# Optimization experiments

Measured on AMD Instinct MI355X. Metric: run time of the kernel, lower is better.

## Reference

```python
import jax, jax.numpy as jnp
import numpy as np

N, K, C, S = 40000, 16, 128, 8  # points, neighbors, channels, share_planes
EPS = 1e-5


def _bn(x, g, b, m, v):
    # eval-mode BatchNorm1d over the channel (last) axis
    return (x - m) * (g * jax.lax.rsqrt(v + EPS)) + b


def _forward(xyz, feats, Wq, bq, Wk, bk, Wv, bv, Wp1, bp1, p_gamma, p_beta, p_mean, p_var,
             Wp2, bp2, w_gamma, w_beta, w_mean, w_var, Ww1, bw1, w1_gamma, w1_beta,
             w1_mean, w1_var, Ww2, bw2, nei_ind):
    x = feats[0]          # (N, C)
    pos = xyz[0]          # (N, 3)
    idx = nei_ind[0]      # (N, K)

    q = x @ Wq + bq                      # (N, C)
    kf = (x @ Wk + bk)[idx]              # (N, K, C) neighbor gather
    vf = (x @ Wv + bv)[idx]              # (N, K, C)

    d = pos[idx] - pos[:, None, :]       # (N, K, 3) relative positions
    # linear_p: Linear_BN(3,3) -> ReLU -> Linear(3, C)
    p = jax.nn.relu(_bn(d @ Wp1 + bp1, p_gamma, p_beta, p_mean, p_var)) @ Wp2 + bp2  # (N, K, C)

    # mid_planes == out_planes, so the view(...,1,mid).sum(2) is an identity reshape
    w = kf - q[:, None, :] + p           # (N, K, C)
    w = _bn(w, w_gamma, w_beta, w_mean, w_var)  # bn_w over channels
    # linear_w: ReLU -> Linear_BN(C, C//S) -> ReLU -> Linear(C//S, C//S)
    w = jax.nn.relu(_bn(jax.nn.relu(w) @ Ww1 + bw1, w1_gamma, w1_beta, w1_mean, w1_var)) @ Ww2 + bw2  # (N, K, C//S)
    w = jax.nn.softmax(w, axis=1)        # softmax over K neighbors

    # grouped-channel weighted sum over neighbors
    agg = ((vf + p).reshape(N, K, S, C // S) * w[:, :, None, :]).sum(axis=1).reshape(N, C)

    # shortcut is Identity (in_planes == out_planes); broadcast over batch dim like torch
    return jax.nn.leaky_relu(agg[None, :, :] + feats, negative_slope=0.1)  # (1, N, C)


def setup_inputs() -> dict:
    key = jax.random.key(0)
    ks = jax.random.split(key, 16)
    f32 = jnp.float32

    def w(k, shape, scale):
        return jax.random.normal(k, shape, dtype=f32) * scale

    return {
        "xyz": jax.random.uniform(ks[0], (1, N, 3), dtype=f32),
        "feats": jax.random.normal(ks[1], (1, N, C), dtype=f32),
        "nei_ind": jax.random.randint(ks[2], (1, N, K), 0, N, dtype=jnp.int32),
        "Wq": w(ks[3], (C, C), C ** -0.5), "bq": jnp.zeros((C,), f32),
        "Wk": w(ks[4], (C, C), C ** -0.5), "bk": jnp.zeros((C,), f32),
        "Wv": w(ks[5], (C, C), C ** -0.5), "bv": jnp.zeros((C,), f32),
        "Wp1": w(ks[6], (3, 3), 0.5), "bp1": jnp.zeros((3,), f32),
        "p_gamma": jnp.ones((3,), f32), "p_beta": jnp.zeros((3,), f32),
        "p_mean": w(ks[7], (3,), 0.1), "p_var": jnp.ones((3,), f32),
        "Wp2": w(ks[8], (3, C), 0.5), "bp2": jnp.zeros((C,), f32),
        "w_gamma": jnp.ones((C,), f32), "w_beta": jnp.zeros((C,), f32),
        "w_mean": w(ks[9], (C,), 0.1), "w_var": jnp.ones((C,), f32),
        "Ww1": w(ks[10], (C, C // S), C ** -0.5), "bw1": jnp.zeros((C // S,), f32),
        "w1_gamma": jnp.ones((C // S,), f32), "w1_beta": jnp.zeros((C // S,), f32),
        "w1_mean": w(ks[11], (C // S,), 0.1), "w1_var": jnp.ones((C // S,), f32),
        "Ww2": w(ks[12], (C // S, C // S), (C // S) ** -0.5), "bw2": jnp.zeros((C // S,), f32),
    }


def reference(xyz, feats, nei_ind, Wq, bq, Wk, bk, Wv, bv, Wp1, bp1, p_gamma, p_beta,
              p_mean, p_var, Wp2, bp2, w_gamma, w_beta, w_mean, w_var, Ww1, bw1,
              w1_gamma, w1_beta, w1_mean, w1_var, Ww2, bw2):
    return _forward(xyz, feats, Wq, bq, Wk, bk, Wv, bv, Wp1, bp1, p_gamma, p_beta,
                    p_mean, p_var, Wp2, bp2, w_gamma, w_beta, w_mean, w_var, Ww1, bw1,
                    w1_gamma, w1_beta, w1_mean, w1_var, Ww2, bw2, nei_ind)
```

## Files before the change

kernel.cpp:

```cpp
#include <hip/hip_runtime.h>
#include <stdint.h>

#define N_PTS 40000
#define KNBR  16
#define CH    128
#define EPSV  1e-5f

typedef __attribute__((ext_vector_type(4))) float f32x4;
typedef __attribute__((ext_vector_type(8))) short bf16x8;

__device__ __forceinline__ float bf2f(ushort u) {
    union { uint32_t i; float f; } x; x.i = ((uint32_t)u) << 16; return x.f;
}
__device__ __forceinline__ float bflo(uint32_t u) {
    union { uint32_t i; float f; } x; x.i = u << 16; return x.f;
}
__device__ __forceinline__ float bfhi(uint32_t u) {
    union { uint32_t i; float f; } x; x.i = u & 0xffff0000u; return x.f;
}
__device__ __forceinline__ ushort f2bf(float f) {
    union { float f; uint32_t i; } x; x.f = f;
    uint32_t i = x.i;
    i += 0x7fffu + ((i >> 16) & 1u);
    return (ushort)(i >> 16);
}

#if __has_builtin(__builtin_amdgcn_cvt_pk_bf16_f32)
typedef __bf16 bf16x2v __attribute__((ext_vector_type(2)));
__device__ __forceinline__ uint32_t pack2(float a, float b) {
    union { bf16x2v v; uint32_t u; } x;
    x.v = __builtin_amdgcn_cvt_pk_bf16_f32(a, b);
    return x.u;
}
#else
__device__ __forceinline__ uint32_t pack2(float a, float b) {
    return (uint32_t)f2bf(a) | ((uint32_t)f2bf(b) << 16);
}
#endif

template <bool BF> struct IO;
template <> struct IO<true> {
    static __device__ __forceinline__ float  ld (const void* p, int i) { return bf2f(((const ushort*)p)[i]); }
    static __device__ __forceinline__ float2 ld2(const void* p, int i) { const uint32_t u = ((const uint32_t*)p)[i]; return make_float2(bflo(u), bfhi(u)); }
    static __device__ __forceinline__ ushort ldbf(const void* p, int i) { return ((const ushort*)p)[i]; }
    static __device__ __forceinline__ void   st2(void* p, int i, float a, float b) { ((uint32_t*)p)[i] = pack2(a, b); }
};
template <> struct IO<false> {
    static __device__ __forceinline__ float  ld (const void* p, int i) { return ((const float*)p)[i]; }
    static __device__ __forceinline__ float2 ld2(const void* p, int i) { return ((const float2*)p)[i]; }
    static __device__ __forceinline__ ushort ldbf(const void* p, int i) { return f2bf(((const float*)p)[i]); }
    static __device__ __forceinline__ void   st2(void* p, int i, float a, float b) { ((float2*)p)[i] = make_float2(a, b); }
};

__device__ __forceinline__ bool detect_bf16(const void* w_var) {
    return (*(const uint32_t*)w_var & 0xffffu) != 0u;
}

template <bool BF>
__device__ void wtrans_body(const void* Wq, const void* Wk, const void* Wv,
                            ushort* wt)
{
    const int m    = blockIdx.x >> 4;
    const int part = blockIdx.x & 15;
    const void* W = (m == 0) ? Wq : (m == 1) ? Wk : Wv;
    const int base = part * 1024 + threadIdx.x * 4;
    #pragma unroll
    for (int e = 0; e < 4; ++e) {
        const int idx = base + e;
        const int k = idx >> 7;
        const int c = idx & 127;
        wt[m * 16384 + c * 128 + k] = IO<BF>::ldbf(W, idx);
    }
}

__global__ __launch_bounds__(256) void wtrans_kernel(
    const void* Wq, const void* Wk, const void* Wv, const void* w_var_probe,
    ushort* wt)
{
    if (detect_bf16(w_var_probe)) wtrans_body<true >(Wq, Wk, Wv, wt);
    else                          wtrans_body<false>(Wq, Wk, Wv, wt);
}

#define PROJ_BLOCKS 1250
template <bool BF>
__device__ void proj_body(
    const void* feats, const ushort* __restrict__ wt,
    const void* bq, const void* bk, const void* bv,
    uint32_t* qws, uint4* kvws,
    ushort* xs, uint32_t* qs_s, uint32_t* kv_s)
{
    const int tid  = threadIdx.x;
    const int l    = tid & 63;
    const int w    = tid >> 6;
    const int t    = l & 15;
    const int quad = l >> 4;
    const int cq   = w;

    const void* bsrc[3] = { bq, bk, bv };

    bf16x8 afrag[3][4];
    float  bias[3][4];
    #pragma unroll
    for (int m = 0; m < 3; ++m) {
        const ushort* wtm = wt + m * 16384 + (cq * 16 + t) * 128 + quad * 8;
        #pragma unroll
        for (int s = 0; s < 4; ++s)
            afrag[m][s] = *(const bf16x8*)(wtm + s * 32);
        #pragma unroll
        for (int r = 0; r < 4; ++r)
            bias[m][r] = IO<BF>::ld(bsrc[m], cq * 16 + quad * 4 + r);
    }

    #pragma unroll 1
    for (int n = 0; n < 2; ++n) {
        const int tt = blockIdx.x + PROJ_BLOCKS * n;
        const int p0 = tt * 16;

        {
            const int r   = tid >> 5;
            const int c32 = tid & 31;
            if (BF) {
                const ushort4 v = *(const ushort4*)((const ushort*)feats + (p0 + r) * CH + c32 * 4);
                *(ushort4*)&xs[r * 136 + c32 * 4] = v;
            } else {
                const float4 v = *(const float4*)((const float*)feats + (p0 + r) * CH + c32 * 4);
                ushort4 o;
                o.x = f2bf(v.x); o.y = f2bf(v.y); o.z = f2bf(v.z); o.w = f2bf(v.w);
                *(ushort4*)&xs[r * 136 + c32 * 4] = o;
            }
        }
        __syncthreads();

        bf16x8 bfr[4];
        #pragma unroll
        for (int s = 0; s < 4; ++s)
            bfr[s] = *(const bf16x8*)&xs[t * 136 + quad * 8 + s * 32];

        f32x4 acc[3];
        #pragma unroll
        for (int m = 0; m < 3; ++m) {
            acc[m] = f32x4{ bias[m][0], bias[m][1], bias[m][2], bias[m][3] };
            #pragma unroll
            for (int s = 0; s < 4; ++s)
                acc[m] = __builtin_amdgcn_mfma_f32_16x16x32_bf16(afrag[m][s], bfr[s], acc[m], 0, 0, 0);
        }

        const int m16 = cq * 4 + quad;
        uint2 qo;
        qo.x = pack2(acc[0][0], acc[0][1]);
        qo.y = pack2(acc[0][2], acc[0][3]);
        *(uint2*)&qs_s[t * 66 + m16 * 2] = qo;
        uint4 kv;
        kv.x = pack2(acc[1][0], acc[1][1]);
        kv.y = pack2(acc[2][0], acc[2][1]);
        kv.z = pack2(acc[1][2], acc[1][3]);
        kv.w = pack2(acc[2][2], acc[2][3]);
        *(uint4*)&kv_s[t * 132 + m16 * 4] = kv;
        __syncthreads();

        {
            const int r = tid >> 5;
            const int u = tid & 31;
            ((uint2*)qws)[(p0 + r) * 32 + u] = *(const uint2*)&qs_s[r * 66 + u * 2];
            kvws[(p0 + r) * 32 + u]          = *(const uint4*)&kv_s[r * 132 + u * 4];
        }
    }
}

__global__ __launch_bounds__(512) void proj_kernel(
    const void* feats, const ushort* __restrict__ wt,
    const void* bq, const void* bk, const void* bv, const void* w_var_probe,
    uint32_t* qws, uint4* kvws)
{
    __shared__ ushort   xs[16 * 136];
    __shared__ uint32_t qs_s[16 * 66];
    __shared__ uint32_t kv_s[16 * 132];
    if (detect_bf16(w_var_probe))
        proj_body<true >(feats, wt, bq, bk, bv, qws, kvws, xs, qs_s, kv_s);
    else
        proj_body<false>(feats, wt, bq, bk, bv, qws, kvws, xs, qs_s, kv_s);
}

template <bool BF>
__device__ void attn_body(
    const void* xyz, const void* feats, const int* __restrict__ nei,
    const uint32_t* __restrict__ qws, const uint2* __restrict__ kvws,
    const void* Wp1, const void* bp1, const void* p_gamma, const void* p_beta,
    const void* p_mean, const void* p_var, const void* Wp2, const void* bp2,
    const void* w_gamma, const void* w_beta, const void* w_mean, const void* w_var,
    const void* Ww1, const void* bw1, const void* w1_gamma, const void* w1_beta,
    const void* w1_mean, const void* w1_var, const void* Ww2, const void* bw2,
    void* out, ushort* wbuf, ushort* ubuf, float* wsm, float* hlds,
    int i0, int l)
{
    const int t = l & 15;
    const int quad = l >> 4;

    float A1[3][3], C1[3];
    #pragma unroll
    for (int b = 0; b < 3; ++b) {
        const float sb = IO<BF>::ld(p_gamma, b) * rsqrtf(IO<BF>::ld(p_var, b) + EPSV);
        C1[b] = (IO<BF>::ld(bp1, b) - IO<BF>::ld(p_mean, b)) * sb + IO<BF>::ld(p_beta, b);
        #pragma unroll
        for (int a = 0; a < 3; ++a) A1[a][b] = IO<BF>::ld(Wp1, a * 3 + b) * sb;
    }

    const float2 vg = IO<BF>::ld2(w_gamma, l);
    const float2 vb = IO<BF>::ld2(w_beta, l);
    const float2 vm = IO<BF>::ld2(w_mean, l);
    const float2 vv = IO<BF>::ld2(w_var, l);
    const float scw0 = vg.x * rsqrtf(vv.x + EPSV);
    const float scw1 = vg.y * rsqrtf(vv.y + EPSV);
    const float shw0 = vb.x - vm.x * scw0;
    const float shw1 = vb.y - vm.y * scw1;

    float wp2c[3][2];
    #pragma unroll
    for (int r = 0; r < 3; ++r) {
        const float2 u = IO<BF>::ld2(Wp2, r * 64 + l);
        wp2c[r][0] = u.x; wp2c[r][1] = u.y;
    }
    const float2 vbp2 = IO<BF>::ld2(bp2, l);
    const float bp20 = vbp2.x, bp21 = vbp2.y;

    bf16x8 bfrag1[4];
    #pragma unroll
    for (int s = 0; s < 4; ++s)
        #pragma unroll
        for (int kk = 0; kk < 8; ++kk) {
            const int k = s * 32 + quad * 8 + kk;
            bfrag1[s][kk] = (short)IO<BF>::ldbf(Ww1, k * 16 + t);
        }
    bf16x8 bfrag2;
    #pragma unroll
    for (int kk = 0; kk < 8; ++kk) {
        const int k = quad * 8 + kk;
        bfrag2[kk] = (quad < 2) ? (short)IO<BF>::ldbf(Ww2, k * 16 + t) : (short)0;
    }

    const float s1t  = IO<BF>::ld(w1_gamma, t) * rsqrtf(IO<BF>::ld(w1_var, t) + EPSV);
    const float sh1t = IO<BF>::ld(w1_beta, t) - IO<BF>::ld(w1_mean, t) * s1t;
    const float bw1t = IO<BF>::ld(bw1, t);
    const float bw2t = IO<BF>::ld(bw2, t);

    #pragma unroll 1
    for (int pp = 0; pp < 4; ++pp) {
        const int i = i0 + pp;

        const uint32_t uq = qws[i * 64 + l];
        const float qs0 = shw0 - bflo(uq) * scw0;
        const float qs1 = shw1 - bfhi(uq) * scw1;

        const float pix = IO<BF>::ld(xyz, i * 3 + 0);
        const float piy = IO<BF>::ld(xyz, i * 3 + 1);
        const float piz = IO<BF>::ld(xyz, i * 3 + 2);

        const int vnj = nei[i * KNBR + t];
        const float ndx = IO<BF>::ld(xyz, vnj * 3 + 0) - pix;
        const float ndy = IO<BF>::ld(xyz, vnj * 3 + 1) - piy;
        const float ndz = IO<BF>::ld(xyz, vnj * 3 + 2) - piz;
        const float hh0 = fmaxf(0.f, ndx * A1[0][0] + ndy * A1[1][0] + ndz * A1[2][0] + C1[0]);
        const float hh1 = fmaxf(0.f, ndx * A1[0][1] + ndy * A1[1][1] + ndz * A1[2][1] + C1[1]);
        const float hh2 = fmaxf(0.f, ndx * A1[0][2] + ndy * A1[1][2] + ndz * A1[2][2] + C1[2]);
        if (quad == 0)
            *(float4*)&hlds[t * 4] = make_float4(hh0, hh1, hh2, 0.f);

        int njs[KNBR];
        #pragma unroll
        for (int j = 0; j < KNBR; ++j) njs[j] = nei[i * KNBR + j];
        uint2 kv[KNBR];
        #pragma unroll
        for (int j = 0; j < KNBR; ++j) kv[j] = kvws[njs[j] * 64 + l];

        float vfp0[KNBR], vfp1[KNBR];
        #pragma unroll
        for (int j = 0; j < KNBR; ++j) {
            const float4 h = *(const float4*)&hlds[j * 4];
            const float p0 = h.x * wp2c[0][0] + h.y * wp2c[1][0] + h.z * wp2c[2][0] + bp20;
            const float p1 = h.x * wp2c[0][1] + h.y * wp2c[1][1] + h.z * wp2c[2][1] + bp21;
            vfp0[j] = bflo(kv[j].y) + p0;
            vfp1[j] = bfhi(kv[j].y) + p1;
            const float w0 = fmaxf(0.f, fmaf(bflo(kv[j].x) + p0, scw0, qs0));
            const float w1 = fmaxf(0.f, fmaf(bfhi(kv[j].x) + p1, scw1, qs1));
            ((uint32_t*)wbuf)[j * 68 + l] = pack2(w0, w1);
        }

        f32x4 acc1 = { bw1t, bw1t, bw1t, bw1t };
        const ushort* arow = &wbuf[t * 136 + quad * 8];
        #pragma unroll
        for (int s = 0; s < 4; ++s) {
            const bf16x8 afrag = *(const bf16x8*)(arow + s * 32);
            acc1 = __builtin_amdgcn_mfma_f32_16x16x32_bf16(afrag, bfrag1[s], acc1, 0, 0, 0);
        }
        #pragma unroll
        for (int r = 0; r < 4; ++r) {
            const float u = fmaxf(0.f, acc1[r] * s1t + sh1t);
            ubuf[(quad * 4 + r) * 24 + t] = f2bf(u);
        }

        f32x4 acc2 = { bw2t, bw2t, bw2t, bw2t };
        bf16x8 afrag2;
        if (quad < 2) {
            afrag2 = *(const bf16x8*)(&ubuf[t * 24 + quad * 8]);
        } else {
            #pragma unroll
            for (int kk = 0; kk < 8; ++kk) afrag2[kk] = 0;
        }
        acc2 = __builtin_amdgcn_mfma_f32_16x16x32_bf16(afrag2, bfrag2, acc2, 0, 0, 0);

        float z0 = acc2[0], z1 = acc2[1], z2 = acc2[2], z3 = acc2[3];
        float mx = fmaxf(fmaxf(z0, z1), fmaxf(z2, z3));
        mx = fmaxf(mx, __shfl_xor(mx, 16));
        mx = fmaxf(mx, __shfl_xor(mx, 32));
        const float e0 = __expf(z0 - mx), e1 = __expf(z1 - mx);
        const float e2 = __expf(z2 - mx), e3 = __expf(z3 - mx);
        float ssum = e0 + e1 + e2 + e3;
        ssum += __shfl_xor(ssum, 16);
        ssum += __shfl_xor(ssum, 32);
        const float inv = 1.0f / ssum;
        wsm[(quad * 4 + 0) * 18 + t] = e0 * inv;
        wsm[(quad * 4 + 1) * 18 + t] = e1 * inv;
        wsm[(quad * 4 + 2) * 18 + t] = e2 * inv;
        wsm[(quad * 4 + 3) * 18 + t] = e3 * inv;

        const int t0 = (2 * l) & 15;
        float agg0 = 0.f, agg1 = 0.f;
        #pragma unroll
        for (int j = 0; j < KNBR; ++j) {
            const float2 wp = *(const float2*)&wsm[j * 18 + t0];
            agg0 = fmaf(vfp0[j], wp.x, agg0);
            agg1 = fmaf(vfp1[j], wp.y, agg1);
        }
        const float2 xf = IO<BF>::ld2(feats, i * 64 + l);
        float o0 = agg0 + xf.x;
        float o1 = agg1 + xf.y;
        o0 = o0 > 0.f ? o0 : 0.1f * o0;
        o1 = o1 > 0.f ? o1 : 0.1f * o1;
        IO<BF>::st2(out, i * 64 + l, o0, o1);
    }
}

__global__ __launch_bounds__(256) void attn_kernel(
    const void* xyz, const void* feats, const int* __restrict__ nei,
    const uint32_t* __restrict__ qws, const uint2* __restrict__ kvws,
    const void* Wp1, const void* bp1, const void* p_gamma, const void* p_beta,
    const void* p_mean, const void* p_var, const void* Wp2, const void* bp2,
    const void* w_gamma, const void* w_beta, const void* w_mean, const void* w_var,
    const void* Ww1, const void* bw1, const void* w1_gamma, const void* w1_beta,
    const void* w1_mean, const void* w1_var, const void* Ww2, const void* bw2,
    void* out)
{
    __shared__ ushort wbuf[4][16 * 136];
    __shared__ ushort ubuf[4][16 * 24];
    __shared__ float  wsm [4][16 * 18];
    __shared__ float  hlds[4][16 * 4];

    const int wave = threadIdx.x >> 6;
    const int l    = threadIdx.x & 63;
    const int i0   = blockIdx.x * 16 + wave * 4;

    if (detect_bf16(w_var))
        attn_body<true >(xyz, feats, nei, qws, kvws, Wp1, bp1, p_gamma, p_beta,
                         p_mean, p_var, Wp2, bp2, w_gamma, w_beta, w_mean, w_var,
                         Ww1, bw1, w1_gamma, w1_beta, w1_mean, w1_var, Ww2, bw2,
                         out, wbuf[wave], ubuf[wave], wsm[wave], hlds[wave], i0, l);
    else
        attn_body<false>(xyz, feats, nei, qws, kvws, Wp1, bp1, p_gamma, p_beta,
                         p_mean, p_var, Wp2, bp2, w_gamma, w_beta, w_mean, w_var,
                         Ww1, bw1, w1_gamma, w1_beta, w1_mean, w1_var, Ww2, bw2,
                         out, wbuf[wave], ubuf[wave], wsm[wave], hlds[wave], i0, l);
}

extern "C" void kernel_launch(void* const* d_in, const int* in_sizes, int n_in,
                              void* d_out, int out_size, void* d_ws, size_t ws_size,
                              hipStream_t stream) {
    const void* xyz     = d_in[0];
    const void* feats   = d_in[1];
    const int*  nei     = (const int*)d_in[2];
    const void* Wq      = d_in[3];
    const void* bq      = d_in[4];
    const void* Wk      = d_in[5];
    const void* bk      = d_in[6];
    const void* Wv      = d_in[7];
    const void* bv      = d_in[8];
    const void* Wp1     = d_in[9];
    const void* bp1     = d_in[10];
    const void* p_gamma = d_in[11];
    const void* p_beta  = d_in[12];
    const void* p_mean  = d_in[13];
    const void* p_var   = d_in[14];
    const void* Wp2     = d_in[15];
    const void* bp2     = d_in[16];
    const void* w_gamma = d_in[17];
    const void* w_beta  = d_in[18];
    const void* w_mean  = d_in[19];
    const void* w_var   = d_in[20];
    const void* Ww1     = d_in[21];
    const void* bw1     = d_in[22];
    const void* w1_gamma= d_in[23];
    const void* w1_beta = d_in[24];
    const void* w1_mean = d_in[25];
    const void* w1_var  = d_in[26];
    const void* Ww2     = d_in[27];
    const void* bw2     = d_in[28];

    uint32_t* qws  = (uint32_t*)d_ws;
    uint4*    kvws = (uint4*)(qws + (size_t)N_PTS * 64);

    const size_t base = (size_t)N_PTS * 64 * 4 + (size_t)N_PTS * 32 * 16;
    ushort* wt = (ws_size >= base + 3 * 16384 * sizeof(ushort))
               ? (ushort*)((char*)d_ws + base)
               : (ushort*)d_out;

    wtrans_kernel<<<48, 256, 0, stream>>>(Wq, Wk, Wv, w_var, wt);
    proj_kernel<<<PROJ_BLOCKS, 512, 0, stream>>>(feats, wt, bq, bk, bv, w_var,
                                                 qws, kvws);
    attn_kernel<<<N_PTS / 16, 256, 0, stream>>>(xyz, feats, nei, qws, (const uint2*)kvws,
                                          Wp1, bp1, p_gamma, p_beta, p_mean, p_var,
                                          Wp2, bp2, w_gamma, w_beta, w_mean, w_var,
                                          Ww1, bw1, w1_gamma, w1_beta, w1_mean, w1_var,
                                          Ww2, bw2, d_out);
}
```

Baseline: 211.6 us.

## Pack attention math into float2 vectors, alias LDS buffers, cut register pressure

The per-channel-pair arithmetic is rewritten with float2 vector types so the compiler can emit packed FP32 instructions. Instead of holding two float arrays of value features plus positional encoding across the softmax, the kernel keeps the packed bf16 value words and recomputes the positional term in the aggregation loop. BN/linear constants are forced scalar with readfirstlane. The ubuf and wsm scratch areas now alias the per-wave wbuf region, with a stride of 17. Together these aim to lower VGPR and LDS use so more waves fit per CU, at the cost of extra ALU work and reliance on in-order LDS access within a wave for the aliasing to be safe.

After: 214.9 us. Within noise of the previous version (+1.6%).

```diff
diff --git a/kernel.cpp b/kernel.cpp
--- a/kernel.cpp
+++ b/kernel.cpp
@@ -7,6 +7,7 @@
 #define EPSV  1e-5f
 
 typedef __attribute__((ext_vector_type(4))) float f32x4;
+typedef __attribute__((ext_vector_type(2))) float f32x2;
 typedef __attribute__((ext_vector_type(8))) short bf16x8;
 
 __device__ __forceinline__ float bf2f(ushort u) {
@@ -23,6 +24,22 @@
     uint32_t i = x.i;
     i += 0x7fffu + ((i >> 16) & 1u);
     return (ushort)(i >> 16);
+}
+__device__ __forceinline__ f32x2 unpk2(uint32_t u) {
+    f32x2 r; r.x = bflo(u); r.y = bfhi(u); return r;
+}
+__device__ __forceinline__ f32x2 vmax2(f32x2 a, f32x2 b) {
+#if __has_builtin(__builtin_elementwise_max)
+    return __builtin_elementwise_max(a, b);
+#else
+    f32x2 r; r.x = fmaxf(a.x, b.x); r.y = fmaxf(a.y, b.y); return r;
+#endif
+}
+
+__device__ __forceinline__ float rfl(float x) {
+    union { float f; int i; } u; u.f = x;
+    u.i = __builtin_amdgcn_readfirstlane(u.i);
+    return u.f;
 }
 
 #if __has_builtin(__builtin_amdgcn_cvt_pk_bf16_f32)
@@ -200,28 +217,29 @@
     #pragma unroll
     for (int b = 0; b < 3; ++b) {
         const float sb = IO<BF>::ld(p_gamma, b) * rsqrtf(IO<BF>::ld(p_var, b) + EPSV);
-        C1[b] = (IO<BF>::ld(bp1, b) - IO<BF>::ld(p_mean, b)) * sb + IO<BF>::ld(p_beta, b);
-        #pragma unroll
-        for (int a = 0; a < 3; ++a) A1[a][b] = IO<BF>::ld(Wp1, a * 3 + b) * sb;
+        C1[b] = rfl((IO<BF>::ld(bp1, b) - IO<BF>::ld(p_mean, b)) * sb + IO<BF>::ld(p_beta, b));
+        #pragma unroll
+        for (int a = 0; a < 3; ++a) A1[a][b] = rfl(IO<BF>::ld(Wp1, a * 3 + b) * sb);
     }
 
     const float2 vg = IO<BF>::ld2(w_gamma, l);
     const float2 vb = IO<BF>::ld2(w_beta, l);
     const float2 vm = IO<BF>::ld2(w_mean, l);
     const float2 vv = IO<BF>::ld2(w_var, l);
-    const float scw0 = vg.x * rsqrtf(vv.x + EPSV);
-    const float scw1 = vg.y * rsqrtf(vv.y + EPSV);
-    const float shw0 = vb.x - vm.x * scw0;
-    const float shw1 = vb.y - vm.y * scw1;
-
-    float wp2c[3][2];
+    f32x2 scwv, shwv;
+    scwv.x = vg.x * rsqrtf(vv.x + EPSV);
+    scwv.y = vg.y * rsqrtf(vv.y + EPSV);
+    shwv.x = vb.x - vm.x * scwv.x;
+    shwv.y = vb.y - vm.y * scwv.y;
+
+    f32x2 wp2v[3];
     #pragma unroll
     for (int r = 0; r < 3; ++r) {
         const float2 u = IO<BF>::ld2(Wp2, r * 64 + l);
-        wp2c[r][0] = u.x; wp2c[r][1] = u.y;
+        wp2v[r].x = u.x; wp2v[r].y = u.y;
     }
     const float2 vbp2 = IO<BF>::ld2(bp2, l);
-    const float bp20 = vbp2.x, bp21 = vbp2.y;
+    f32x2 bp2v; bp2v.x = vbp2.x; bp2v.y = vbp2.y;
 
     bf16x8 bfrag1[4];
     #pragma unroll
@@ -248,8 +266,7 @@
         const int i = i0 + pp;
 
         const uint32_t uq = qws[i * 64 + l];
-        const float qs0 = shw0 - bflo(uq) * scw0;
-        const float qs1 = shw1 - bfhi(uq) * scw1;
+        const f32x2 qsv = shwv - unpk2(uq) * scwv;
 
         const float pix = IO<BF>::ld(xyz, i * 3 + 0);
         const float piy = IO<BF>::ld(xyz, i * 3 + 1);
@@ -272,17 +289,15 @@
         #pragma unroll
         for (int j = 0; j < KNBR; ++j) kv[j] = kvws[njs[j] * 64 + l];
 
-        float vfp0[KNBR], vfp1[KNBR];
+        uint32_t vpk[KNBR];
         #pragma unroll
         for (int j = 0; j < KNBR; ++j) {
             const float4 h = *(const float4*)&hlds[j * 4];
-            const float p0 = h.x * wp2c[0][0] + h.y * wp2c[1][0] + h.z * wp2c[2][0] + bp20;
-            const float p1 = h.x * wp2c[0][1] + h.y * wp2c[1][1] + h.z * wp2c[2][1] + bp21;
-            vfp0[j] = bflo(kv[j].y) + p0;
-            vfp1[j] = bfhi(kv[j].y) + p1;
-            const float w0 = fmaxf(0.f, fmaf(bflo(kv[j].x) + p0, scw0, qs0));
-            const float w1 = fmaxf(0.f, fmaf(bfhi(kv[j].x) + p1, scw1, qs1));
-            ((uint32_t*)wbuf)[j * 68 + l] = pack2(w0, w1);
+            const f32x2 pv = h.x * wp2v[0] + h.y * wp2v[1] + h.z * wp2v[2] + bp2v;
+            vpk[j] = kv[j].y;
+            const f32x2 wv = vmax2((unpk2(kv[j].x) + pv) * scwv + qsv,
+                                   f32x2{0.f, 0.f});
+            ((uint32_t*)wbuf)[j * 68 + l] = pack2(wv.x, wv.y);
         }
 
         f32x4 acc1 = { bw1t, bw1t, bw1t, bw1t };
@@ -318,25 +333,26 @@
         ssum += __shfl_xor(ssum, 16);
         ssum += __shfl_xor(ssum, 32);
         const float inv = 1.0f / ssum;
-        wsm[(quad * 4 + 0) * 18 + t] = e0 * inv;
-        wsm[(quad * 4 + 1) * 18 + t] = e1 * inv;
-        wsm[(quad * 4 + 2) * 18 + t] = e2 * inv;
-        wsm[(quad * 4 + 3) * 18 + t] = e3 * inv;
+        wsm[(quad * 4 + 0) * 17 + t] = e0 * inv;
+        wsm[(quad * 4 + 1) * 17 + t] = e1 * inv;
+        wsm[(quad * 4 + 2) * 17 + t] = e2 * inv;
+        wsm[(quad * 4 + 3) * 17 + t] = e3 * inv;
 
         const int t0 = (2 * l) & 15;
-        float agg0 = 0.f, agg1 = 0.f;
+        f32x2 aggv = { 0.f, 0.f };
         #pragma unroll
         for (int j = 0; j < KNBR; ++j) {
-            const float2 wp = *(const float2*)&wsm[j * 18 + t0];
-            agg0 = fmaf(vfp0[j], wp.x, agg0);
-            agg1 = fmaf(vfp1[j], wp.y, agg1);
+            f32x2 wp;
+            wp.x = wsm[j * 17 + t0];
+            wp.y = wsm[j * 17 + t0 + 1];
+            const float4 h = *(const float4*)&hlds[j * 4];
+            const f32x2 pv = h.x * wp2v[0] + h.y * wp2v[1] + h.z * wp2v[2] + bp2v;
+            aggv += (unpk2(vpk[j]) + pv) * wp;
         }
         const float2 xf = IO<BF>::ld2(feats, i * 64 + l);
-        float o0 = agg0 + xf.x;
-        float o1 = agg1 + xf.y;
-        o0 = o0 > 0.f ? o0 : 0.1f * o0;
-        o1 = o1 > 0.f ? o1 : 0.1f * o1;
-        IO<BF>::st2(out, i * 64 + l, o0, o1);
+        f32x2 ov; ov.x = aggv.x + xf.x; ov.y = aggv.y + xf.y;
+        ov = vmax2(ov, 0.1f * ov);
+        IO<BF>::st2(out, i * 64 + l, ov.x, ov.y);
     }
 }
 
@@ -351,24 +367,26 @@
     void* out)
 {
     __shared__ ushort wbuf[4][16 * 136];
-    __shared__ ushort ubuf[4][16 * 24];
-    __shared__ float  wsm [4][16 * 18];
     __shared__ float  hlds[4][16 * 4];
 
     const int wave = threadIdx.x >> 6;
     const int l    = threadIdx.x & 63;
     const int i0   = blockIdx.x * 16 + wave * 4;
+
+    ushort* wb  = wbuf[wave];
+    ushort* ub  = wb;
+    float*  wsm = (float*)((char*)wb + 1024);
 
     if (detect_bf16(w_var))
         attn_body<true >(xyz, feats, nei, qws, kvws, Wp1, bp1, p_gamma, p_beta,
                          p_mean, p_var, Wp2, bp2, w_gamma, w_beta, w_mean, w_var,
                          Ww1, bw1, w1_gamma, w1_beta, w1_mean, w1_var, Ww2, bw2,
-                         out, wbuf[wave], ubuf[wave], wsm[wave], hlds[wave], i0, l);
+                         out, wb, ub, wsm, hlds[wave], i0, l);
     else
         attn_body<false>(xyz, feats, nei, qws, kvws, Wp1, bp1, p_gamma, p_beta,
                          p_mean, p_var, Wp2, bp2, w_gamma, w_beta, w_mean, w_var,
                          Ww1, bw1, w1_gamma, w1_beta, w1_mean, w1_var, Ww2, bw2,
-                         out, wbuf[wave], ubuf[wave], wsm[wave], hlds[wave], i0, l);
+                         out, wb, ub, wsm, hlds[wave], i0, l);
 }
 
 extern "C" void kernel_launch(void* const* d_in, const int* in_sizes, int n_in,
```
